# Optimization experiments

Measured on AMD Instinct MI355X. Metric: run time of the kernel, lower is better.

## Reference

```python
import jax, jax.numpy as jnp
import numpy as np

V, M, N, C, H, OUT = 50000, 16, 8, 8, 4, 256
DK = OUT // H  # 64


def setup_inputs() -> dict:
    key = jax.random.key(0)
    ks = jax.random.split(key, 9)
    return {
        "x": jax.random.normal(ks[0], (V, C * N), dtype=jnp.float32),
        "neighbors": jax.random.randint(ks[1], (V, M), 0, V, dtype=jnp.int64),
        "parallel_transport_matrices": jax.random.normal(ks[2], (V, M, N, N), dtype=jnp.float32),
        "rel_pos_u": jax.random.normal(ks[3], (V, M, 2), dtype=jnp.float32),
        "W_Q_w": jax.random.normal(ks[4], (OUT, C * N), dtype=jnp.float32) * 0.05,
        "W_Q_b": jnp.zeros((OUT,), dtype=jnp.float32),
        "W_K_w": jax.random.normal(ks[5], (OUT, C * N), dtype=jnp.float32) * 0.05,
        "W_K_b": jnp.zeros((OUT,), dtype=jnp.float32),
        "kernel_bases": jax.random.normal(ks[6], (6, N, N), dtype=jnp.float32),
        "kernel_coeffs": jax.random.normal(ks[7], (H, 6), dtype=jnp.float32),
    }


def reference(x, neighbors, parallel_transport_matrices, rel_pos_u,
              W_Q_w, W_Q_b, W_K_w, W_K_b, kernel_bases, kernel_coeffs):
    Nv = x.shape[0]
    # gather neighbor features and split channel axis: [V, M, C, N]
    x_neigh = x[neighbors].reshape(Nv, M, C, N)
    # parallel transport: [V,M,N,N] x [V,M,C,N] -> [V,M,N,C]
    f_prime = jnp.einsum('vnoj,vnpj->vnop', parallel_transport_matrices, x_neigh)
    f_prime_flat = f_prime.reshape(Nv, M, C * N)  # row-major flatten (as torch)
    # queries / keys
    Q = (x @ W_Q_w.T + W_Q_b).reshape(Nv, H, DK)
    K = (f_prime_flat @ W_K_w.T + W_K_b).reshape(Nv, M, H, DK)
    scores = jnp.einsum('vhd,vnhd->vnh', Q, K) / np.float32(np.sqrt(DK))
    attn = jax.nn.softmax(scores, axis=1)  # softmax over neighbors
    # learned value transform from fixed kernel bases: [H,N,N]
    W_V = jnp.einsum('hb,bij->hij', kernel_coeffs, kernel_bases)
    f_split = f_prime_flat.reshape(Nv, M, C, N)
    # values: [V,M,H,C,N] -> [V,M,H,C*N]
    values = jnp.einsum('hij,vncj->vnhci', W_V, f_split).reshape(Nv, M, H, C * N)
    out = jnp.einsum('vnh,vnhd->vhd', attn, values)
    return out.reshape(Nv, H * C * N)
```

## Files before the change

### kernel.cpp

```cpp
#include <hip/hip_runtime.h>
#include <hip/hip_bf16.h>

#define NV 50000


typedef _Float16 h2_t __attribute__((ext_vector_type(2)));
typedef _Float16 f16x4 __attribute__((ext_vector_type(4)));
typedef _Float16 f16x8 __attribute__((ext_vector_type(8)));
typedef float f32x4 __attribute__((ext_vector_type(4)));

#if defined(__has_builtin)
#if __has_builtin(__builtin_amdgcn_fdot2)
#define HAVE_FDOT2 1
#endif
#endif

__device__ __forceinline__ float fdot2f(h2_t a, h2_t b, float c) {
#ifdef HAVE_FDOT2
  return __builtin_amdgcn_fdot2(a, b, c, false);
#else
  return fmaf((float)a.x, (float)b.x, fmaf((float)a.y, (float)b.y, c));
#endif
}
__device__ __forceinline__ h2_t u2h(unsigned u) {
  union { unsigned u; h2_t h; } c; c.u = u; return c.h;
}
__device__ __forceinline__ unsigned pk2(float a, float b) {
  auto v = __builtin_amdgcn_cvt_pkrtz(a, b);
  union { decltype(v) h; unsigned u; } c; c.h = v; return c.u;
}
__device__ __forceinline__ f16x8 u4h8(uint4 u) {
  union { uint4 u; f16x8 h; } c; c.u = u; return c.h;
}
__device__ __forceinline__ f16x4 u2h4(uint2 u) {
  union { uint2 u; f16x4 h; } c; c.u = u; return c.h;
}
__device__ __forceinline__ void lds_fence() {
  asm volatile("s_waitcnt lgkmcnt(0)" ::: "memory");
  __builtin_amdgcn_sched_barrier(0);
}

__global__ void prep_kernel(const float* __restrict__ WQ, const float* __restrict__ WQb,
                            const float* __restrict__ WK,
                            const float* __restrict__ bases, const float* __restrict__ coeffs,
                            const float* __restrict__ x,
                            unsigned* __restrict__ AhTs, float* __restrict__ rbar,
                            unsigned* __restrict__ wvh, unsigned* __restrict__ xh) {
  if (blockIdx.x < 32) {
    int ep = blockIdx.x;
    int od = threadIdx.x;
    int h = od >> 6, d = od & 63;
    int e0 = ep * 2;
    float s0 = 0.f, s1 = 0.f;
#pragma unroll 4
    for (int k = 0; k < 64; ++k) {
      float wk = WK[(h * 64 + k) * 64 + d];
      s0 += WQ[(h * 64 + k) * 64 + e0] * wk;
      s1 += WQ[(h * 64 + k) * 64 + e0 + 1] * wk;
    }
    AhTs[((ep >> 2) * 256 + od) * 4 + (ep & 3)] = pk2(s0 * 0.125f, s1 * 0.125f);
    if (ep == 0) {
      float r = 0.f;
      for (int k = 0; k < 64; ++k) r += WQb[h * 64 + k] * WK[(h * 64 + k) * 64 + d];
      rbar[od] = r * 0.125f;
      if (od < 128) {
        int i = od >> 4, hh = (od >> 2) & 3, jp = od & 3;
        float w0 = 0.f, w1 = 0.f;
        for (int b = 0; b < 6; ++b) {
          w0 += coeffs[hh * 6 + b] * bases[b * 64 + i * 8 + 2 * jp];
          w1 += coeffs[hh * 6 + b] * bases[b * 64 + i * 8 + 2 * jp + 1];
        }
        wvh[od] = pk2(w0, w1);
      }
    }
  } else {
    int idx = (blockIdx.x - 32) * 256 + threadIdx.x;
    if (idx < NV * 8) {
      float4 a = ((const float4*)x)[idx * 2];
      float4 b = ((const float4*)x)[idx * 2 + 1];
      uint4 o;
      o.x = pk2(a.x, a.y);
      o.y = pk2(a.z, a.w);
      o.z = pk2(b.x, b.y);
      o.w = pk2(b.z, b.w);
      ((uint4*)xh)[idx] = o;
    }
  }
}

__global__ __launch_bounds__(256, 4) void attn_kernel(
    const unsigned* __restrict__ xh, const int* __restrict__ nbr,
    const float* __restrict__ P, const unsigned* __restrict__ AhTs,
    const float* __restrict__ rbar, const unsigned* __restrict__ wvh,
    float* __restrict__ out) {
  __shared__ __align__(16) _Float16 TA[4][1152];
  __shared__ __align__(16) _Float16 TB[4][1152];
  __shared__ __align__(16) _Float16 TC[4][1152];
  __shared__ __align__(16) _Float16 q16[8][256];

  const int t = threadIdx.x;
  const int w = t >> 6, lane = t & 63;
  const int v0 = blockIdx.x * 8;
  const int va = v0 + w, vb = v0 + 4 + w;
  const int c_ep = lane >> 3, i_ep = lane & 7;
  const int m_ = lane & 15, dg = lane >> 4;
  const char* xhb = (const char*)xh;
  _Float16* g16w = &q16[w][0];

  const int pm = lane >> 4;
  const int po = ((lane & 15) >> 1) * 8 + 4 * (lane & 1);

  int nbA0 = nbr[(size_t)va * 16 + (lane >> 3)];
  int nbA1 = nbr[(size_t)va * 16 + 8 + (lane >> 3)];
  int nbB0 = nbr[(size_t)vb * 16 + (lane >> 3)];
  int nbB1 = nbr[(size_t)vb * 16 + 8 + (lane >> 3)];
  uint4 xA0 = *(const uint4*)(xhb + (size_t)nbA0 * 128 + (lane & 7) * 16);
  uint4 xA1 = *(const uint4*)(xhb + (size_t)nbA1 * 128 + (lane & 7) * 16);
  uint4 xB0 = *(const uint4*)(xhb + (size_t)nbB0 * 128 + (lane & 7) * 16);
  uint4 xB1 = *(const uint4*)(xhb + (size_t)nbB1 * 128 + (lane & 7) * 16);

  f32x4 a0, a1, a2, a3, b0, b1, b2, b3;
  {
    const f32x4* PgA = (const f32x4*)(P + (size_t)va * 1024);
    const f32x4* PgB = (const f32x4*)(P + (size_t)vb * 1024);
    a0 = PgA[lane];
    a1 = PgA[64 + lane];
    a2 = PgA[128 + lane];
    a3 = PgA[192 + lane];
    b0 = PgB[lane];
    b1 = PgB[64 + lane];
    b2 = PgB[128 + lane];
    b3 = PgB[192 + lane];
  }

  {
    uint2 u0, u1, u2, u3;
    u0.x = pk2(a0[0], a0[1]); u0.y = pk2(a0[2], a0[3]);
    u1.x = pk2(a1[0], a1[1]); u1.y = pk2(a1[2], a1[3]);
    u2.x = pk2(a2[0], a2[1]); u2.y = pk2(a2[2], a2[3]);
    u3.x = pk2(a3[0], a3[1]); u3.y = pk2(a3[2], a3[3]);
    *(uint2*)&TA[w][(0 + pm) * 72 + po]  = u0;
    *(uint2*)&TA[w][(4 + pm) * 72 + po]  = u1;
    *(uint2*)&TA[w][(8 + pm) * 72 + po]  = u2;
    *(uint2*)&TA[w][(12 + pm) * 72 + po] = u3;
    *(uint4*)&TB[w][(lane >> 3) * 72 + (lane & 7) * 8] = xA0;
    *(uint4*)&TB[w][((lane >> 3) + 8) * 72 + (lane & 7) * 8] = xA1;
  }

  float rbq[4];
#pragma unroll
  for (int tt = 0; tt < 4; ++tt) rbq[tt] = rbar[w * 64 + tt * 16 + (lane & 15)];

  {
    const int od0 = w * 64;
    uint4 bu[2][4];
#pragma unroll
    for (int s = 0; s < 2; ++s)
#pragma unroll
      for (int tt = 0; tt < 4; ++tt)
        bu[s][tt] = *(const uint4*)&AhTs[((s * 4 + (lane >> 4)) * 256 + od0 + tt * 16 + (lane & 15)) * 4];

    const uint4* xr = (const uint4*)(xh + (size_t)(v0 + (lane & 7)) * 32);
    f16x8 af0 = u4h8(xr[(lane >> 4)]);
    f16x8 af1 = u4h8(xr[4 + (lane >> 4)]);
    f32x4 acc[4];
#pragma unroll
    for (int tt = 0; tt < 4; ++tt) acc[tt] = (f32x4){0.f, 0.f, 0.f, 0.f};
    __builtin_amdgcn_s_setprio(1);
#pragma unroll
    for (int tt = 0; tt < 4; ++tt)
#pragma unroll
      for (int s = 0; s < 2; ++s)
        acc[tt] = __builtin_amdgcn_mfma_f32_16x16x32_f16(s ? af1 : af0, u4h8(bu[s][tt]),
                                                         acc[tt], 0, 0, 0);
    __builtin_amdgcn_s_setprio(0);
    if (lane < 32) {
#pragma unroll
      for (int tt = 0; tt < 4; ++tt)
#pragma unroll
        for (int reg = 0; reg < 4; ++reg)
          q16[(lane >> 4) * 4 + reg][od0 + tt * 16 + (lane & 15)] =
              (_Float16)(acc[tt][reg] + rbq[tt]);
    }
  }
  __syncthreads();

  const int hb = (lane & 15) & 3;
  f16x8 bqa0 = u4h8(*(const uint4*)&q16[w][hb * 64 + dg * 8]);
  f16x8 bqa1 = u4h8(*(const uint4*)&q16[w][hb * 64 + 32 + dg * 8]);
  f16x8 bqb0 = u4h8(*(const uint4*)&q16[4 + w][hb * 64 + dg * 8]);
  f16x8 bqb1 = u4h8(*(const uint4*)&q16[4 + w][hb * 64 + 32 + dg * 8]);
  uint4 wq[4];
#pragma unroll
  for (int h = 0; h < 4; ++h) wq[h] = *(const uint4*)&wvh[i_ep * 16 + h * 4];

  const int rl = lane & 15, kg = lane >> 4;

  uint4 A0a, A1a;
  f16x4 eba;
  {
    uint4 Plo = *(const uint4*)&TA[w][m_ * 72 + dg * 8];
    uint4 Phi = *(const uint4*)&TA[w][m_ * 72 + (dg + 4) * 8];
    float fr0[8], fr1[8];
    __builtin_amdgcn_s_setprio(1);
#pragma unroll
    for (int c = 0; c < 8; ++c) {
      uint4 Xu = *(const uint4*)&TB[w][m_ * 72 + c * 8];
      fr0[c] = fdot2f(u2h(Plo.x), u2h(Xu.x),
               fdot2f(u2h(Plo.y), u2h(Xu.y),
               fdot2f(u2h(Plo.z), u2h(Xu.z),
               fdot2f(u2h(Plo.w), u2h(Xu.w), 0.f))));
      fr1[c] = fdot2f(u2h(Phi.x), u2h(Xu.x),
               fdot2f(u2h(Phi.y), u2h(Xu.y),
               fdot2f(u2h(Phi.z), u2h(Xu.z),
               fdot2f(u2h(Phi.w), u2h(Xu.w), 0.f))));
    }
    __builtin_amdgcn_s_setprio(0);
    A0a.x = pk2(fr0[0], fr0[1]); A0a.y = pk2(fr0[2], fr0[3]);
    A0a.z = pk2(fr0[4], fr0[5]); A0a.w = pk2(fr0[6], fr0[7]);
    A1a.x = pk2(fr1[0], fr1[1]); A1a.y = pk2(fr1[2], fr1[3]);
    A1a.z = pk2(fr1[4], fr1[5]); A1a.w = pk2(fr1[6], fr1[7]);
    f32x4 sac = (f32x4){0.f, 0.f, 0.f, 0.f};
    sac = __builtin_amdgcn_mfma_f32_16x16x32_f16(u4h8(A0a), bqa0, sac, 0, 0, 0);
    sac = __builtin_amdgcn_mfma_f32_16x16x32_f16(u4h8(A1a), bqa1, sac, 0, 0, 0);
    float e0 = __expf(sac[0]), e1 = __expf(sac[1]);
    float e2 = __expf(sac[2]), e3 = __expf(sac[3]);
    float pp = (e0 + e1) + (e2 + e3);
    pp += __shfl_xor(pp, 16);
    pp += __shfl_xor(pp, 32);
    float is = __builtin_amdgcn_rcpf(pp);
    uint2 eu;
    eu.x = pk2(e0 * is, e1 * is);
    eu.y = pk2(e2 * is, e3 * is);
    eba = u2h4(eu);
  }
  lds_fence();

  *(uint4*)&TC[w][m_ * 72 + dg * 8] = A0a;
  *(uint4*)&TC[w][m_ * 72 + 32 + dg * 8] = A1a;
  {
    uint2 u0, u1, u2, u3;
    u0.x = pk2(b0[0], b0[1]); u0.y = pk2(b0[2], b0[3]);
    u1.x = pk2(b1[0], b1[1]); u1.y = pk2(b1[2], b1[3]);
    u2.x = pk2(b2[0], b2[1]); u2.y = pk2(b2[2], b2[3]);
    u3.x = pk2(b3[0], b3[1]); u3.y = pk2(b3[2], b3[3]);
    *(uint2*)&TA[w][(0 + pm) * 72 + po]  = u0;
    *(uint2*)&TA[w][(4 + pm) * 72 + po]  = u1;
    *(uint2*)&TA[w][(8 + pm) * 72 + po]  = u2;
    *(uint2*)&TA[w][(12 + pm) * 72 + po] = u3;
    *(uint4*)&TB[w][(lane >> 3) * 72 + (lane & 7) * 8] = xB0;
    *(uint4*)&TB[w][((lane >> 3) + 8) * 72 + (lane & 7) * 8] = xB1;
  }
  lds_fence();

  __builtin_amdgcn_s_setprio(1);
#pragma unroll
  for (int b2i = 0; b2i < 4; ++b2i) {
    f16x4 ga;
#pragma unroll
    for (int tt = 0; tt < 4; ++tt)
      ga[tt] = TC[w][(kg * 4 + tt) * 72 + b2i * 16 + rl];
    f32x4 zg = (f32x4){0.f, 0.f, 0.f, 0.f};
    f32x4 gacc = __builtin_amdgcn_mfma_f32_16x16x16f16(ga, eba, zg, 0, 0, 0);
    if (rl < 4) {
      uint2 gv;
      gv.x = pk2(gacc[0], gacc[1]);
      gv.y = pk2(gacc[2], gacc[3]);
      *(uint2*)&g16w[rl * 64 + b2i * 16 + kg * 4] = gv;
    }
  }
  __builtin_amdgcn_s_setprio(0);

  uint4 A0b, A1b;
  f16x4 ebb;
  {
    uint4 Plo = *(const uint4*)&TA[w][m_ * 72 + dg * 8];
    uint4 Phi = *(const uint4*)&TA[w][m_ * 72 + (dg + 4) * 8];
    float fr0[8], fr1[8];
    __builtin_amdgcn_s_setprio(1);
#pragma unroll
    for (int c = 0; c < 8; ++c) {
      uint4 Xu = *(const uint4*)&TB[w][m_ * 72 + c * 8];
      fr0[c] = fdot2f(u2h(Plo.x), u2h(Xu.x),
               fdot2f(u2h(Plo.y), u2h(Xu.y),
               fdot2f(u2h(Plo.z), u2h(Xu.z),
               fdot2f(u2h(Plo.w), u2h(Xu.w), 0.f))));
      fr1[c] = fdot2f(u2h(Phi.x), u2h(Xu.x),
               fdot2f(u2h(Phi.y), u2h(Xu.y),
               fdot2f(u2h(Phi.z), u2h(Xu.z),
               fdot2f(u2h(Phi.w), u2h(Xu.w), 0.f))));
    }
    __builtin_amdgcn_s_setprio(0);
    A0b.x = pk2(fr0[0], fr0[1]); A0b.y = pk2(fr0[2], fr0[3]);
    A0b.z = pk2(fr0[4], fr0[5]); A0b.w = pk2(fr0[6], fr0[7]);
    A1b.x = pk2(fr1[0], fr1[1]); A1b.y = pk2(fr1[2], fr1[3]);
    A1b.z = pk2(fr1[4], fr1[5]); A1b.w = pk2(fr1[6], fr1[7]);
    f32x4 sac = (f32x4){0.f, 0.f, 0.f, 0.f};
    sac = __builtin_amdgcn_mfma_f32_16x16x32_f16(u4h8(A0b), bqb0, sac, 0, 0, 0);
    sac = __builtin_amdgcn_mfma_f32_16x16x32_f16(u4h8(A1b), bqb1, sac, 0, 0, 0);
    float e0 = __expf(sac[0]), e1 = __expf(sac[1]);
    float e2 = __expf(sac[2]), e3 = __expf(sac[3]);
    float pp = (e0 + e1) + (e2 + e3);
    pp += __shfl_xor(pp, 16);
    pp += __shfl_xor(pp, 32);
    float is = __builtin_amdgcn_rcpf(pp);
    uint2 eu;
    eu.x = pk2(e0 * is, e1 * is);
    eu.y = pk2(e2 * is, e3 * is);
    ebb = u2h4(eu);
  }
  lds_fence();

#pragma unroll
  for (int h = 0; h < 4; ++h) {
    uint4 gq = *(const uint4*)&g16w[h * 64 + c_ep * 8];
    float oacc = fdot2f(u2h(wq[h].x), u2h(gq.x),
                 fdot2f(u2h(wq[h].y), u2h(gq.y),
                 fdot2f(u2h(wq[h].z), u2h(gq.z),
                 fdot2f(u2h(wq[h].w), u2h(gq.w), 0.f))));
    __builtin_nontemporal_store(oacc, &out[(size_t)va * 256 + h * 64 + lane]);
  }
  *(uint4*)&TC[w][m_ * 72 + dg * 8] = A0b;
  *(uint4*)&TC[w][m_ * 72 + 32 + dg * 8] = A1b;
  lds_fence();

  __builtin_amdgcn_s_setprio(1);
#pragma unroll
  for (int b2i = 0; b2i < 4; ++b2i) {
    f16x4 ga;
#pragma unroll
    for (int tt = 0; tt < 4; ++tt)
      ga[tt] = TC[w][(kg * 4 + tt) * 72 + b2i * 16 + rl];
    f32x4 zg = (f32x4){0.f, 0.f, 0.f, 0.f};
    f32x4 gacc = __builtin_amdgcn_mfma_f32_16x16x16f16(ga, ebb, zg, 0, 0, 0);
    if (rl < 4) {
      uint2 gv;
      gv.x = pk2(gacc[0], gacc[1]);
      gv.y = pk2(gacc[2], gacc[3]);
      *(uint2*)&g16w[rl * 64 + b2i * 16 + kg * 4] = gv;
    }
  }
  __builtin_amdgcn_s_setprio(0);
  lds_fence();

#pragma unroll
  for (int h = 0; h < 4; ++h) {
    uint4 gq = *(const uint4*)&g16w[h * 64 + c_ep * 8];
    float oacc = fdot2f(u2h(wq[h].x), u2h(gq.x),
                 fdot2f(u2h(wq[h].y), u2h(gq.y),
                 fdot2f(u2h(wq[h].z), u2h(gq.z),
                 fdot2f(u2h(wq[h].w), u2h(gq.w), 0.f))));
    __builtin_nontemporal_store(oacc, &out[(size_t)vb * 256 + h * 64 + lane]);
  }
}

extern "C" void kernel_launch(void* const* d_in, const int* in_sizes, int n_in,
                              void* d_out, int out_size, void* d_ws, size_t ws_size,
                              hipStream_t stream) {
  const float* x      = (const float*)d_in[0];
  const int*   nbr    = (const int*)d_in[1];
  const float* P      = (const float*)d_in[2];
  const float* WQ     = (const float*)d_in[4];
  const float* WQb    = (const float*)d_in[5];
  const float* WK     = (const float*)d_in[6];
  const float* bases  = (const float*)d_in[8];
  const float* coeffs = (const float*)d_in[9];

  unsigned* AhTs = (unsigned*)d_ws;
  float* rbar   = (float*)((char*)d_ws + 32768);
  unsigned* wvh = (unsigned*)((char*)d_ws + 33792);
  unsigned* xh  = (unsigned*)((char*)d_ws + 34816);
  float* out    = (float*)d_out;

  hipLaunchKernelGGL(prep_kernel, dim3(32 + (NV * 8 + 255) / 256), dim3(256), 0, stream,
                     WQ, WQb, WK, bases, coeffs, x, AhTs, rbar, wvh, xh);
  hipLaunchKernelGGL(attn_kernel, dim3(NV / 8), dim3(256), 0, stream,
                     xh, nbr, P, AhTs, rbar, wvh, out);
}
```

Before: 65.45 us.

## Process sixteen vertices per block with software-pipelined staging of P and gathers

Measured after the change: 69.42 us. 1.06x slower.

```diff
diff --git a/kernel.cpp b/kernel.cpp
--- a/kernel.cpp
+++ b/kernel.cpp
@@ -96,12 +96,12 @@
   __shared__ __align__(16) _Float16 TA[4][1152];
   __shared__ __align__(16) _Float16 TB[4][1152];
   __shared__ __align__(16) _Float16 TC[4][1152];
-  __shared__ __align__(16) _Float16 q16[8][256];
+  __shared__ __align__(16) _Float16 q16[16][256];
 
   const int t = threadIdx.x;
   const int w = t >> 6, lane = t & 63;
-  const int v0 = blockIdx.x * 8;
-  const int va = v0 + w, vb = v0 + 4 + w;
+  const int v0 = blockIdx.x * 16;
+  const int va = v0 + w, vb = v0 + 4 + w, vc = v0 + 8 + w, vd = v0 + 12 + w;
   const int c_ep = lane >> 3, i_ep = lane & 7;
   const int m_ = lane & 15, dg = lane >> 4;
   const char* xhb = (const char*)xh;
@@ -109,96 +109,39 @@
 
   const int pm = lane >> 4;
   const int po = ((lane & 15) >> 1) * 8 + 4 * (lane & 1);
+  const int rl = lane & 15, kg = lane >> 4;
+  const int hb = (lane & 15) & 3;
 
   int nbA0 = nbr[(size_t)va * 16 + (lane >> 3)];
   int nbA1 = nbr[(size_t)va * 16 + 8 + (lane >> 3)];
   int nbB0 = nbr[(size_t)vb * 16 + (lane >> 3)];
   int nbB1 = nbr[(size_t)vb * 16 + 8 + (lane >> 3)];
-  uint4 xA0 = *(const uint4*)(xhb + (size_t)nbA0 * 128 + (lane & 7) * 16);
-  uint4 xA1 = *(const uint4*)(xhb + (size_t)nbA1 * 128 + (lane & 7) * 16);
-  uint4 xB0 = *(const uint4*)(xhb + (size_t)nbB0 * 128 + (lane & 7) * 16);
-  uint4 xB1 = *(const uint4*)(xhb + (size_t)nbB1 * 128 + (lane & 7) * 16);
-
-  f32x4 a0, a1, a2, a3, b0, b1, b2, b3;
-  {
-    const f32x4* PgA = (const f32x4*)(P + (size_t)va * 1024);
-    const f32x4* PgB = (const f32x4*)(P + (size_t)vb * 1024);
-    a0 = PgA[lane];
-    a1 = PgA[64 + lane];
-    a2 = PgA[128 + lane];
-    a3 = PgA[192 + lane];
-    b0 = PgB[lane];
-    b1 = PgB[64 + lane];
-    b2 = PgB[128 + lane];
-    b3 = PgB[192 + lane];
-  }
-
-  {
-    uint2 u0, u1, u2, u3;
-    u0.x = pk2(a0[0], a0[1]); u0.y = pk2(a0[2], a0[3]);
-    u1.x = pk2(a1[0], a1[1]); u1.y = pk2(a1[2], a1[3]);
-    u2.x = pk2(a2[0], a2[1]); u2.y = pk2(a2[2], a2[3]);
-    u3.x = pk2(a3[0], a3[1]); u3.y = pk2(a3[2], a3[3]);
-    *(uint2*)&TA[w][(0 + pm) * 72 + po]  = u0;
-    *(uint2*)&TA[w][(4 + pm) * 72 + po]  = u1;
-    *(uint2*)&TA[w][(8 + pm) * 72 + po]  = u2;
-    *(uint2*)&TA[w][(12 + pm) * 72 + po] = u3;
-    *(uint4*)&TB[w][(lane >> 3) * 72 + (lane & 7) * 8] = xA0;
-    *(uint4*)&TB[w][((lane >> 3) + 8) * 72 + (lane & 7) * 8] = xA1;
-  }
-
-  float rbq[4];
-#pragma unroll
-  for (int tt = 0; tt < 4; ++tt) rbq[tt] = rbar[w * 64 + tt * 16 + (lane & 15)];
-
-  {
-    const int od0 = w * 64;
-    uint4 bu[2][4];
-#pragma unroll
-    for (int s = 0; s < 2; ++s)
-#pragma unroll
-      for (int tt = 0; tt < 4; ++tt)
-        bu[s][tt] = *(const uint4*)&AhTs[((s * 4 + (lane >> 4)) * 256 + od0 + tt * 16 + (lane & 15)) * 4];
-
-    const uint4* xr = (const uint4*)(xh + (size_t)(v0 + (lane & 7)) * 32);
-    f16x8 af0 = u4h8(xr[(lane >> 4)]);
-    f16x8 af1 = u4h8(xr[4 + (lane >> 4)]);
-    f32x4 acc[4];
-#pragma unroll
-    for (int tt = 0; tt < 4; ++tt) acc[tt] = (f32x4){0.f, 0.f, 0.f, 0.f};
-    __builtin_amdgcn_s_setprio(1);
-#pragma unroll
-    for (int tt = 0; tt < 4; ++tt)
-#pragma unroll
-      for (int s = 0; s < 2; ++s)
-        acc[tt] = __builtin_amdgcn_mfma_f32_16x16x32_f16(s ? af1 : af0, u4h8(bu[s][tt]),
-                                                         acc[tt], 0, 0, 0);
-    __builtin_amdgcn_s_setprio(0);
-    if (lane < 32) {
-#pragma unroll
-      for (int tt = 0; tt < 4; ++tt)
-#pragma unroll
-        for (int reg = 0; reg < 4; ++reg)
-          q16[(lane >> 4) * 4 + reg][od0 + tt * 16 + (lane & 15)] =
-              (_Float16)(acc[tt][reg] + rbq[tt]);
-    }
-  }
-  __syncthreads();
-
-  const int hb = (lane & 15) & 3;
-  f16x8 bqa0 = u4h8(*(const uint4*)&q16[w][hb * 64 + dg * 8]);
-  f16x8 bqa1 = u4h8(*(const uint4*)&q16[w][hb * 64 + 32 + dg * 8]);
-  f16x8 bqb0 = u4h8(*(const uint4*)&q16[4 + w][hb * 64 + dg * 8]);
-  f16x8 bqb1 = u4h8(*(const uint4*)&q16[4 + w][hb * 64 + 32 + dg * 8]);
-  uint4 wq[4];
-#pragma unroll
-  for (int h = 0; h < 4; ++h) wq[h] = *(const uint4*)&wvh[i_ep * 16 + h * 4];
-
-  const int rl = lane & 15, kg = lane >> 4;
-
-  uint4 A0a, A1a;
-  f16x4 eba;
-  {
+  int nbC0 = nbr[(size_t)vc * 16 + (lane >> 3)];
+  int nbC1 = nbr[(size_t)vc * 16 + 8 + (lane >> 3)];
+  int nbD0 = nbr[(size_t)vd * 16 + (lane >> 3)];
+  int nbD1 = nbr[(size_t)vd * 16 + 8 + (lane >> 3)];
+
+  auto loadPackP = [&](const float* base, uint2& q0, uint2& q1, uint2& q2, uint2& q3) {
+    const f32x4* Pg = (const f32x4*)base;
+    f32x4 r0 = Pg[lane], r1 = Pg[64 + lane], r2 = Pg[128 + lane], r3 = Pg[192 + lane];
+    q0.x = pk2(r0[0], r0[1]); q0.y = pk2(r0[2], r0[3]);
+    q1.x = pk2(r1[0], r1[1]); q1.y = pk2(r1[2], r1[3]);
+    q2.x = pk2(r2[0], r2[1]); q2.y = pk2(r2[2], r2[3]);
+    q3.x = pk2(r3[0], r3[1]); q3.y = pk2(r3[2], r3[3]);
+  };
+  auto stagePX = [&](uint2 q0, uint2 q1, uint2 q2, uint2 q3, uint4 x0, uint4 x1) {
+    *(uint2*)&TA[w][(0 + pm) * 72 + po]  = q0;
+    *(uint2*)&TA[w][(4 + pm) * 72 + po]  = q1;
+    *(uint2*)&TA[w][(8 + pm) * 72 + po]  = q2;
+    *(uint2*)&TA[w][(12 + pm) * 72 + po] = q3;
+    *(uint4*)&TB[w][(lane >> 3) * 72 + (lane & 7) * 8] = x0;
+    *(uint4*)&TB[w][((lane >> 3) + 8) * 72 + (lane & 7) * 8] = x1;
+  };
+  auto writeTC = [&](uint4 A0, uint4 A1) {
+    *(uint4*)&TC[w][m_ * 72 + dg * 8] = A0;
+    *(uint4*)&TC[w][m_ * 72 + 32 + dg * 8] = A1;
+  };
+  auto fsm = [&](f16x8 bq0, f16x8 bq1, uint4& A0, uint4& A1) -> f16x4 {
     uint4 Plo = *(const uint4*)&TA[w][m_ * 72 + dg * 8];
     uint4 Phi = *(const uint4*)&TA[w][m_ * 72 + (dg + 4) * 8];
     float fr0[8], fr1[8];
@@ -216,13 +159,13 @@
                fdot2f(u2h(Phi.w), u2h(Xu.w), 0.f))));
     }
     __builtin_amdgcn_s_setprio(0);
-    A0a.x = pk2(fr0[0], fr0[1]); A0a.y = pk2(fr0[2], fr0[3]);
-    A0a.z = pk2(fr0[4], fr0[5]); A0a.w = pk2(fr0[6], fr0[7]);
-    A1a.x = pk2(fr1[0], fr1[1]); A1a.y = pk2(fr1[2], fr1[3]);
-    A1a.z = pk2(fr1[4], fr1[5]); A1a.w = pk2(fr1[6], fr1[7]);
+    A0.x = pk2(fr0[0], fr0[1]); A0.y = pk2(fr0[2], fr0[3]);
+    A0.z = pk2(fr0[4], fr0[5]); A0.w = pk2(fr0[6], fr0[7]);
+    A1.x = pk2(fr1[0], fr1[1]); A1.y = pk2(fr1[2], fr1[3]);
+    A1.z = pk2(fr1[4], fr1[5]); A1.w = pk2(fr1[6], fr1[7]);
     f32x4 sac = (f32x4){0.f, 0.f, 0.f, 0.f};
-    sac = __builtin_amdgcn_mfma_f32_16x16x32_f16(u4h8(A0a), bqa0, sac, 0, 0, 0);
-    sac = __builtin_amdgcn_mfma_f32_16x16x32_f16(u4h8(A1a), bqa1, sac, 0, 0, 0);
+    sac = __builtin_amdgcn_mfma_f32_16x16x32_f16(u4h8(A0), bq0, sac, 0, 0, 0);
+    sac = __builtin_amdgcn_mfma_f32_16x16x32_f16(u4h8(A1), bq1, sac, 0, 0, 0);
     float e0 = __expf(sac[0]), e1 = __expf(sac[1]);
     float e2 = __expf(sac[2]), e3 = __expf(sac[3]);
     float pp = (e0 + e1) + (e2 + e3);
@@ -232,83 +175,110 @@
     uint2 eu;
     eu.x = pk2(e0 * is, e1 * is);
     eu.y = pk2(e2 * is, e3 * is);
-    eba = u2h4(eu);
-  }
-  lds_fence();
-
-  *(uint4*)&TC[w][m_ * 72 + dg * 8] = A0a;
-  *(uint4*)&TC[w][m_ * 72 + 32 + dg * 8] = A1a;
-  {
+    return u2h4(eu);
+  };
+  auto gphase = [&](f16x4 eb) {
+    __builtin_amdgcn_s_setprio(1);
+#pragma unroll
+    for (int b2i = 0; b2i < 4; ++b2i) {
+      f16x4 ga;
+#pragma unroll
+      for (int tt = 0; tt < 4; ++tt)
+        ga[tt] = TC[w][(kg * 4 + tt) * 72 + b2i * 16 + rl];
+      f32x4 zg = (f32x4){0.f, 0.f, 0.f, 0.f};
+      f32x4 gacc = __builtin_amdgcn_mfma_f32_16x16x16f16(ga, eb, zg, 0, 0, 0);
+      if (rl < 4) {
+        uint2 gv;
+        gv.x = pk2(gacc[0], gacc[1]);
+        gv.y = pk2(gacc[2], gacc[3]);
+        *(uint2*)&g16w[rl * 64 + b2i * 16 + kg * 4] = gv;
+      }
+    }
+    __builtin_amdgcn_s_setprio(0);
+  };
+
+  uint4 xA0 = *(const uint4*)(xhb + (size_t)nbA0 * 128 + (lane & 7) * 16);
+  uint4 xA1 = *(const uint4*)(xhb + (size_t)nbA1 * 128 + (lane & 7) * 16);
+  uint4 xB0 = *(const uint4*)(xhb + (size_t)nbB0 * 128 + (lane & 7) * 16);
+  uint4 xB1 = *(const uint4*)(xhb + (size_t)nbB1 * 128 + (lane & 7) * 16);
+  uint2 pb0, pb1, pb2, pb3;
+  loadPackP(P + (size_t)vb * 1024, pb0, pb1, pb2, pb3);
+  {
+    const f32x4* PgA = (const f32x4*)(P + (size_t)va * 1024);
+    f32x4 a0 = PgA[lane], a1 = PgA[64 + lane], a2 = PgA[128 + lane], a3 = PgA[192 + lane];
     uint2 u0, u1, u2, u3;
-    u0.x = pk2(b0[0], b0[1]); u0.y = pk2(b0[2], b0[3]);
-    u1.x = pk2(b1[0], b1[1]); u1.y = pk2(b1[2], b1[3]);
-    u2.x = pk2(b2[0], b2[1]); u2.y = pk2(b2[2], b2[3]);
-    u3.x = pk2(b3[0], b3[1]); u3.y = pk2(b3[2], b3[3]);
-    *(uint2*)&TA[w][(0 + pm) * 72 + po]  = u0;
-    *(uint2*)&TA[w][(4 + pm) * 72 + po]  = u1;
-    *(uint2*)&TA[w][(8 + pm) * 72 + po]  = u2;
-    *(uint2*)&TA[w][(12 + pm) * 72 + po] = u3;
-    *(uint4*)&TB[w][(lane >> 3) * 72 + (lane & 7) * 8] = xB0;
-    *(uint4*)&TB[w][((lane >> 3) + 8) * 72 + (lane & 7) * 8] = xB1;
-  }
-  lds_fence();
-
-  __builtin_amdgcn_s_setprio(1);
-#pragma unroll
-  for (int b2i = 0; b2i < 4; ++b2i) {
-    f16x4 ga;
+    u0.x = pk2(a0[0], a0[1]); u0.y = pk2(a0[2], a0[3]);
+    u1.x = pk2(a1[0], a1[1]); u1.y = pk2(a1[2], a1[3]);
+    u2.x = pk2(a2[0], a2[1]); u2.y = pk2(a2[2], a2[3]);
+    u3.x = pk2(a3[0], a3[1]); u3.y = pk2(a3[2], a3[3]);
+    stagePX(u0, u1, u2, u3, xA0, xA1);
+  }
+
+  float rbq[4];
+#pragma unroll
+  for (int tt = 0; tt < 4; ++tt) rbq[tt] = rbar[w * 64 + tt * 16 + (lane & 15)];
+
+  {
+    const int od0 = w * 64;
+    uint4 bu[2][4];
+#pragma unroll
+    for (int s = 0; s < 2; ++s)
+#pragma unroll
+      for (int tt = 0; tt < 4; ++tt)
+        bu[s][tt] = *(const uint4*)&AhTs[((s * 4 + (lane >> 4)) * 256 + od0 + tt * 16 + (lane & 15)) * 4];
+
+    const uint4* xr = (const uint4*)(xh + (size_t)(v0 + (lane & 15)) * 32);
+    f16x8 af0 = u4h8(xr[(lane >> 4)]);
+    f16x8 af1 = u4h8(xr[4 + (lane >> 4)]);
+    f32x4 acc[4];
+#pragma unroll
+    for (int tt = 0; tt < 4; ++tt) acc[tt] = (f32x4){0.f, 0.f, 0.f, 0.f};
+    __builtin_amdgcn_s_setprio(1);
 #pragma unroll
     for (int tt = 0; tt < 4; ++tt)
-      ga[tt] = TC[w][(kg * 4 + tt) * 72 + b2i * 16 + rl];
-    f32x4 zg = (f32x4){0.f, 0.f, 0.f, 0.f};
-    f32x4 gacc = __builtin_amdgcn_mfma_f32_16x16x16f16(ga, eba, zg, 0, 0, 0);
-    if (rl < 4) {
-      uint2 gv;
-      gv.x = pk2(gacc[0], gacc[1]);
-      gv.y = pk2(gacc[2], gacc[3]);
-      *(uint2*)&g16w[rl * 64 + b2i * 16 + kg * 4] = gv;
-    }
-  }
-  __builtin_amdgcn_s_setprio(0);
-
+#pragma unroll
+      for (int s = 0; s < 2; ++s)
+        acc[tt] = __builtin_amdgcn_mfma_f32_16x16x32_f16(s ? af1 : af0, u4h8(bu[s][tt]),
+                                                         acc[tt], 0, 0, 0);
+    __builtin_amdgcn_s_setprio(0);
+#pragma unroll
+    for (int tt = 0; tt < 4; ++tt)
+#pragma unroll
+      for (int reg = 0; reg < 4; ++reg)
+        q16[(lane >> 4) * 4 + reg][od0 + tt * 16 + (lane & 15)] =
+            (_Float16)(acc[tt][reg] + rbq[tt]);
+  }
+
+  __builtin_amdgcn_sched_barrier(0);
+  uint2 pc0, pc1, pc2, pc3, pd0, pd1, pd2, pd3;
+  loadPackP(P + (size_t)vc * 1024, pc0, pc1, pc2, pc3);
+  loadPackP(P + (size_t)vd * 1024, pd0, pd1, pd2, pd3);
+  __syncthreads();
+
+  f16x8 bqa0 = u4h8(*(const uint4*)&q16[w][hb * 64 + dg * 8]);
+  f16x8 bqa1 = u4h8(*(const uint4*)&q16[w][hb * 64 + 32 + dg * 8]);
+
+  uint4 A0a, A1a;
+  f16x4 eba = fsm(bqa0, bqa1, A0a, A1a);
+  lds_fence();
+
+  writeTC(A0a, A1a);
+  stagePX(pb0, pb1, pb2, pb3, xB0, xB1);
+  uint4 xC0 = *(const uint4*)(xhb + (size_t)nbC0 * 128 + (lane & 7) * 16);
+  uint4 xC1 = *(const uint4*)(xhb + (size_t)nbC1 * 128 + (lane & 7) * 16);
+  lds_fence();
+
+  gphase(eba);
   uint4 A0b, A1b;
   f16x4 ebb;
   {
-    uint4 Plo = *(const uint4*)&TA[w][m_ * 72 + dg * 8];
-    uint4 Phi = *(const uint4*)&TA[w][m_ * 72 + (dg + 4) * 8];
-    float fr0[8], fr1[8];
-    __builtin_amdgcn_s_setprio(1);
-#pragma unroll
-    for (int c = 0; c < 8; ++c) {
-      uint4 Xu = *(const uint4*)&TB[w][m_ * 72 + c * 8];
-      fr0[c] = fdot2f(u2h(Plo.x), u2h(Xu.x),
-               fdot2f(u2h(Plo.y), u2h(Xu.y),
-               fdot2f(u2h(Plo.z), u2h(Xu.z),
-               fdot2f(u2h(Plo.w), u2h(Xu.w), 0.f))));
-      fr1[c] = fdot2f(u2h(Phi.x), u2h(Xu.x),
-               fdot2f(u2h(Phi.y), u2h(Xu.y),
-               fdot2f(u2h(Phi.z), u2h(Xu.z),
-               fdot2f(u2h(Phi.w), u2h(Xu.w), 0.f))));
-    }
-    __builtin_amdgcn_s_setprio(0);
-    A0b.x = pk2(fr0[0], fr0[1]); A0b.y = pk2(fr0[2], fr0[3]);
-    A0b.z = pk2(fr0[4], fr0[5]); A0b.w = pk2(fr0[6], fr0[7]);
-    A1b.x = pk2(fr1[0], fr1[1]); A1b.y = pk2(fr1[2], fr1[3]);
-    A1b.z = pk2(fr1[4], fr1[5]); A1b.w = pk2(fr1[6], fr1[7]);
-    f32x4 sac = (f32x4){0.f, 0.f, 0.f, 0.f};
-    sac = __builtin_amdgcn_mfma_f32_16x16x32_f16(u4h8(A0b), bqb0, sac, 0, 0, 0);
-    sac = __builtin_amdgcn_mfma_f32_16x16x32_f16(u4h8(A1b), bqb1, sac, 0, 0, 0);
-    float e0 = __expf(sac[0]), e1 = __expf(sac[1]);
-    float e2 = __expf(sac[2]), e3 = __expf(sac[3]);
-    float pp = (e0 + e1) + (e2 + e3);
-    pp += __shfl_xor(pp, 16);
-    pp += __shfl_xor(pp, 32);
-    float is = __builtin_amdgcn_rcpf(pp);
-    uint2 eu;
-    eu.x = pk2(e0 * is, e1 * is);
-    eu.y = pk2(e2 * is, e3 * is);
-    ebb = u2h4(eu);
-  }
+    f16x8 bqb0 = u4h8(*(const uint4*)&q16[4 + w][hb * 64 + dg * 8]);
+    f16x8 bqb1 = u4h8(*(const uint4*)&q16[4 + w][hb * 64 + 32 + dg * 8]);
+    ebb = fsm(bqb0, bqb1, A0b, A1b);
+  }
+  uint4 wq[4];
+#pragma unroll
+  for (int h = 0; h < 4; ++h) wq[h] = *(const uint4*)&wvh[i_ep * 16 + h * 4];
   lds_fence();
 
 #pragma unroll
@@ -320,27 +290,20 @@
                  fdot2f(u2h(wq[h].w), u2h(gq.w), 0.f))));
     __builtin_nontemporal_store(oacc, &out[(size_t)va * 256 + h * 64 + lane]);
   }
-  *(uint4*)&TC[w][m_ * 72 + dg * 8] = A0b;
-  *(uint4*)&TC[w][m_ * 72 + 32 + dg * 8] = A1b;
-  lds_fence();
-
-  __builtin_amdgcn_s_setprio(1);
-#pragma unroll
-  for (int b2i = 0; b2i < 4; ++b2i) {
-    f16x4 ga;
-#pragma unroll
-    for (int tt = 0; tt < 4; ++tt)
-      ga[tt] = TC[w][(kg * 4 + tt) * 72 + b2i * 16 + rl];
-    f32x4 zg = (f32x4){0.f, 0.f, 0.f, 0.f};
-    f32x4 gacc = __builtin_amdgcn_mfma_f32_16x16x16f16(ga, ebb, zg, 0, 0, 0);
-    if (rl < 4) {
-      uint2 gv;
-      gv.x = pk2(gacc[0], gacc[1]);
-      gv.y = pk2(gacc[2], gacc[3]);
-      *(uint2*)&g16w[rl * 64 + b2i * 16 + kg * 4] = gv;
-    }
-  }
-  __builtin_amdgcn_s_setprio(0);
+  writeTC(A0b, A1b);
+  stagePX(pc0, pc1, pc2, pc3, xC0, xC1);
+  uint4 xD0 = *(const uint4*)(xhb + (size_t)nbD0 * 128 + (lane & 7) * 16);
+  uint4 xD1 = *(const uint4*)(xhb + (size_t)nbD1 * 128 + (lane & 7) * 16);
+  lds_fence();
+
+  gphase(ebb);
+  uint4 A0c, A1c;
+  f16x4 ebc;
+  {
+    f16x8 bqc0 = u4h8(*(const uint4*)&q16[8 + w][hb * 64 + dg * 8]);
+    f16x8 bqc1 = u4h8(*(const uint4*)&q16[8 + w][hb * 64 + 32 + dg * 8]);
+    ebc = fsm(bqc0, bqc1, A0c, A1c);
+  }
   lds_fence();
 
 #pragma unroll
@@ -351,6 +314,44 @@
                  fdot2f(u2h(wq[h].z), u2h(gq.z),
                  fdot2f(u2h(wq[h].w), u2h(gq.w), 0.f))));
     __builtin_nontemporal_store(oacc, &out[(size_t)vb * 256 + h * 64 + lane]);
+  }
+  writeTC(A0c, A1c);
+  stagePX(pd0, pd1, pd2, pd3, xD0, xD1);
+  lds_fence();
+
+  gphase(ebc);
+  uint4 A0d, A1d;
+  f16x4 ebd;
+  {
+    f16x8 bqd0 = u4h8(*(const uint4*)&q16[12 + w][hb * 64 + dg * 8]);
+    f16x8 bqd1 = u4h8(*(const uint4*)&q16[12 + w][hb * 64 + 32 + dg * 8]);
+    ebd = fsm(bqd0, bqd1, A0d, A1d);
+  }
+  lds_fence();
+
+#pragma unroll
+  for (int h = 0; h < 4; ++h) {
+    uint4 gq = *(const uint4*)&g16w[h * 64 + c_ep * 8];
+    float oacc = fdot2f(u2h(wq[h].x), u2h(gq.x),
+                 fdot2f(u2h(wq[h].y), u2h(gq.y),
+                 fdot2f(u2h(wq[h].z), u2h(gq.z),
+                 fdot2f(u2h(wq[h].w), u2h(gq.w), 0.f))));
+    __builtin_nontemporal_store(oacc, &out[(size_t)vc * 256 + h * 64 + lane]);
+  }
+  writeTC(A0d, A1d);
+  lds_fence();
+
+  gphase(ebd);
+  lds_fence();
+
+#pragma unroll
+  for (int h = 0; h < 4; ++h) {
+    uint4 gq = *(const uint4*)&g16w[h * 64 + c_ep * 8];
+    float oacc = fdot2f(u2h(wq[h].x), u2h(gq.x),
+                 fdot2f(u2h(wq[h].y), u2h(gq.y),
+                 fdot2f(u2h(wq[h].z), u2h(gq.z),
+                 fdot2f(u2h(wq[h].w), u2h(gq.w), 0.f))));
+    __builtin_nontemporal_store(oacc, &out[(size_t)vd * 256 + h * 64 + lane]);
   }
 }
 
@@ -374,6 +375,6 @@
 
   hipLaunchKernelGGL(prep_kernel, dim3(32 + (NV * 8 + 255) / 256), dim3(256), 0, stream,
                      WQ, WQb, WK, bases, coeffs, x, AhTs, rbar, wvh, xh);
-  hipLaunchKernelGGL(attn_kernel, dim3(NV / 8), dim3(256), 0, stream,
+  hipLaunchKernelGGL(attn_kernel, dim3(NV / 16), dim3(256), 0, stream,
                      xh, nbr, P, AhTs, rbar, wvh, out);
 }
```
